# Performance work log

Hardware: AMD Instinct MI355X
Metric: run time of the kernel (lower is better)

The kernel has to match this reference:

```python
import jax, jax.numpy as jnp
import numpy as np

B, S, D = 4, 2048, 1024  # batch, seq_len, d_model (d_in == d_model)


def setup_inputs() -> dict:
    key = jax.random.key(0)
    ks = jax.random.split(key, 9)
    scale = 1.0 / np.sqrt(D)
    return {
        "q": jax.random.normal(ks[0], (B, S, D), jnp.float32),
        "k": jax.random.normal(ks[1], (B, S, D), jnp.float32),
        "v": jax.random.normal(ks[2], (B, S, D), jnp.float32),
        "Wq": jax.random.normal(ks[3], (D, D), jnp.float32) * scale,
        "bq": jnp.zeros((D,), jnp.float32),
        "Wk": jax.random.normal(ks[4], (D, D), jnp.float32) * scale,
        "bk": jnp.zeros((D,), jnp.float32),
        "Wv": jax.random.normal(ks[5], (D, D), jnp.float32) * scale,
        "bv": jnp.zeros((D,), jnp.float32),
    }


def reference(q, k, v, Wq, bq, Wk, bk, Wv, bv):
    query = q @ Wq + bq                      # [B, S, D]
    key_p = k @ Wk + bk                      # [B, S, D]
    value = v @ Wv + bv                      # [B, S, D]
    inv_sqrt_d = 1.0 / jnp.sqrt(jnp.asarray(D, query.dtype))
    scores = jnp.einsum('bqd,bkd->bqk', query, key_p) * inv_sqrt_d  # [B, S, S]
    w = jax.nn.softmax(scores, axis=-1)
    return jnp.einsum('bqk,bkd->bqd', w, value)  # [B, S, D]
```

## Files before the change

kernel.cpp:

```cpp
#include <hip/hip_runtime.h>
#include <math.h>


using short8  = __attribute__((ext_vector_type(8))) short;
using floatx4 = __attribute__((ext_vector_type(4))) float;

__device__ __forceinline__ unsigned short f2bf(float f) {
    union { float f; unsigned u; } x; x.f = f;
    return (unsigned short)((x.u + 0x8000u) >> 16);
}

__device__ __forceinline__ void gload_lds16(const unsigned short* g, unsigned short* l) {
    __builtin_amdgcn_global_load_lds(
        (const __attribute__((address_space(1))) unsigned int*)g,
        (__attribute__((address_space(3))) unsigned int*)l, 16, 0, 0);
}

__global__ __launch_bounds__(256) void prep(
    const float* __restrict__ q, const float* __restrict__ k, const float* __restrict__ v,
    const float* __restrict__ W0, const float* __restrict__ W1, const float* __restrict__ W2,
    unsigned short* __restrict__ qkvbf, unsigned short* __restrict__ Wt)
{
    __shared__ float tile[32][33];
    const int id = blockIdx.x;
    const int t  = threadIdx.x;
    if (id < 24576) {
        const int z  = id >> 13;
        const int xb = id & 8191;
        const float* x = (z == 0) ? q : (z == 1) ? k : v;
        const size_t i = ((size_t)xb * 256 + t) * 4;
        const float4 a = *(const float4*)(x + i);
        ushort4 p = { f2bf(a.x), f2bf(a.y), f2bf(a.z), f2bf(a.w) };
        *(ushort4*)(qkvbf + (size_t)z * 8192 * 1024 + i) = p;
    } else {
        const int idt = id - 24576;
        const int z  = idt >> 10;
        const int r  = idt & 1023;
        const int bx = (r & 31) * 32;
        const int by = (r >> 5) * 32;
        const float* W = (z == 0) ? W0 : (z == 1) ? W1 : W2;
        unsigned short* o = Wt + (size_t)z * 1024 * 1024;
        const int tx = t & 31;
        const int ty = (t >> 5) * 4;
        #pragma unroll
        for (int rr = 0; rr < 4; ++rr)
            tile[ty + rr][tx] = W[(size_t)(by + ty + rr) * 1024 + bx + tx];
        __syncthreads();
        #pragma unroll
        for (int rr = 0; rr < 4; ++rr)
            o[(size_t)(bx + ty + rr) * 1024 + by + tx] = f2bf(tile[tx][ty + rr]);
    }
}

#define KLOOP_BODY(gA, lda, gB, ldb, Kdim)                                        \
    for (int k0 = 0; k0 < (Kdim); k0 += 64) {                                     \
        gload_lds16(gA + k0,                    lA);                              \
        gload_lds16(gA + 64 * (lda) + k0,       lA + 2048);                       \
        gload_lds16(gA + k0 + 32,               lA + 4096);                       \
        gload_lds16(gA + 64 * (lda) + k0 + 32,  lA + 6144);                       \
        gload_lds16(gB + k0,                    lB);                              \
        gload_lds16(gB + 64 * (ldb) + k0,       lB + 2048);                       \
        gload_lds16(gB + k0 + 32,               lB + 4096);                       \
        gload_lds16(gB + 64 * (ldb) + k0 + 32,  lB + 6144);                       \
        __syncthreads();                                                          \
        _Pragma("unroll")                                                         \
        for (int h = 0; h < 2; ++h) {                                             \
            short8 af[4], bfr[4];                                                 \
            _Pragma("unroll")                                                     \
            for (int i = 0; i < 4; ++i)                                           \
                af[i] = *(const short8*)&As[h * 4096 + (wm + i * 16 + l15) * 32 + quad * 8]; \
            _Pragma("unroll")                                                     \
            for (int j = 0; j < 4; ++j)                                           \
                bfr[j] = *(const short8*)&Bs[h * 4096 + (wn + j * 16 + l15) * 32 + quad * 8]; \
            _Pragma("unroll")                                                     \
            for (int i = 0; i < 4; ++i)                                           \
                _Pragma("unroll")                                                 \
                for (int j = 0; j < 4; ++j)                                       \
                    acc[i][j] = __builtin_amdgcn_mfma_f32_16x16x32_bf16(          \
                        af[i], bfr[j], acc[i][j], 0, 0, 0);                       \
        }                                                                         \
        __syncthreads();                                                          \
    }

#define TILE_IDS                                  \
    const int t    = threadIdx.x;                 \
    const int lane = t & 63;                      \
    const int wave = t >> 6;                      \
    const int wm   = (wave & 1) * 64;             \
    const int wn   = (wave >> 1) * 64;            \
    const int l15  = lane & 15;                   \
    const int quad = lane >> 4;                   \
    const int rS = t >> 2;                        \
    const int oS = (t & 3) * 8;

__global__ __launch_bounds__(256) void proj_bf16(
    const unsigned short* __restrict__ Abf,
    const unsigned short* __restrict__ Wt,
    const float* __restrict__ bq, const float* __restrict__ bk, const float* __restrict__ bv,
    unsigned short* __restrict__ Qp, unsigned short* __restrict__ Kp,
    unsigned short* __restrict__ Vpt)
{
    const int id    = blockIdx.x;
    const int xcd   = id & 7;
    const int local = id >> 3;
    const int s     = xcd * 24 + (local >> 3);
    const int n0    = (local & 7) * 128;
    const int z     = s >> 6;
    const int m0    = (s & 63) * 128;

    const unsigned short* A = Abf + (size_t)z * 8192 * 1024;
    const unsigned short* B = Wt  + (size_t)z * 1024 * 1024;
    const float* bias = (z == 0) ? bq : (z == 1) ? bk : bv;

    __shared__ __attribute__((aligned(16))) unsigned short As[2 * 128 * 32];
    __shared__ __attribute__((aligned(16))) unsigned short Bs[2 * 128 * 32];

    TILE_IDS
    const unsigned short* gA = A + (size_t)(m0 + rS) * 1024 + oS;
    const unsigned short* gB = B + (size_t)(n0 + rS) * 1024 + oS;
    unsigned short* lA = &As[t * 8];
    unsigned short* lB = &Bs[t * 8];

    floatx4 acc[4][4] = {};

    KLOOP_BODY(gA, 1024, gB, 1024, 1024)

    #pragma unroll
    for (int j = 0; j < 4; ++j) {
        const int col = n0 + wn + j * 16 + l15;
        const float bv_ = bias[col];
        #pragma unroll
        for (int i = 0; i < 4; ++i) {
            const int row = m0 + wm + i * 16 + quad * 4;
            if (z < 2) {
                unsigned short* C = (z == 0) ? Qp : Kp;
                #pragma unroll
                for (int r = 0; r < 4; ++r)
                    C[(size_t)(row + r) * 1024 + col] = f2bf(acc[i][j][r] + bv_);
            } else {
                ushort4 p = { f2bf(acc[i][j][0] + bv_), f2bf(acc[i][j][1] + bv_),
                              f2bf(acc[i][j][2] + bv_), f2bf(acc[i][j][3] + bv_) };
                *(ushort4*)&Vpt[(size_t)col * 8192 + row] = p;
            }
        }
    }
}

__global__ __launch_bounds__(256) void scores_exp(
    const unsigned short* __restrict__ Qp,
    const unsigned short* __restrict__ Kp,
    unsigned short* __restrict__ Pexp,
    float* __restrict__ rowsum)
{
    const int id    = blockIdx.x;
    const int xcd   = id & 7;
    const int local = id >> 3;
    const int g     = xcd * 128 + local;
    const int z     = g >> 8;
    const int r_    = g & 255;
    const int cm    = r_ >> 6;
    const int rr_   = r_ & 63;
    const int cn    = rr_ >> 4;
    const int inner = rr_ & 15;
    const int m0    = (cm * 4 + (inner >> 2)) * 128;
    const int n0    = (cn * 4 + (inner & 3)) * 128;

    const unsigned short* A = Qp + (size_t)z * 2048 * 1024;
    const unsigned short* B = Kp + (size_t)z * 2048 * 1024;
    unsigned short* P = Pexp + (size_t)z * 2048 * 2048;
    float* rs = rowsum + (size_t)z * 2048;

    __shared__ __attribute__((aligned(16))) unsigned short As[2 * 128 * 32];
    __shared__ __attribute__((aligned(16))) unsigned short Bs[2 * 128 * 32];

    TILE_IDS
    const unsigned short* gA = A + (size_t)(m0 + rS) * 1024 + oS;
    const unsigned short* gB = B + (size_t)(n0 + rS) * 1024 + oS;
    unsigned short* lA = &As[t * 8];
    unsigned short* lB = &Bs[t * 8];

    floatx4 acc[4][4] = {};

    KLOOP_BODY(gA, 1024, gB, 1024, 1024)

    float sm[4][4] = {};
    #pragma unroll
    for (int i = 0; i < 4; ++i) {
        const int rowb = m0 + wm + i * 16 + quad * 4;
        #pragma unroll
        for (int j = 0; j < 4; ++j) {
            const int col = n0 + wn + j * 16 + l15;
            #pragma unroll
            for (int r = 0; r < 4; ++r) {
                const float p = __expf(acc[i][j][r] * 0.03125f);
                sm[i][r] += p;
                P[(size_t)(rowb + r) * 2048 + col] = f2bf(p);
            }
        }
    }
    #pragma unroll
    for (int i = 0; i < 4; ++i)
        #pragma unroll
        for (int r = 0; r < 4; ++r) {
            float s = sm[i][r];
            s += __shfl_xor(s, 1);
            s += __shfl_xor(s, 2);
            s += __shfl_xor(s, 4);
            s += __shfl_xor(s, 8);
            if (l15 == 0)
                atomicAdd(&rs[m0 + wm + i * 16 + quad * 4 + r], s);
        }
}

__global__ __launch_bounds__(256) void pv_norm(
    const unsigned short* __restrict__ Pexp,
    const unsigned short* __restrict__ Vpt,
    const float* __restrict__ rowsum,
    float* __restrict__ out)
{
    const int m0 = blockIdx.y * 128;
    const int n0 = blockIdx.x * 128;
    const int z  = blockIdx.z;

    const unsigned short* A = Pexp + (size_t)z * 2048 * 2048;
    const unsigned short* B = Vpt  + (size_t)z * 2048;
    const float* rs = rowsum + (size_t)z * 2048;
    float* C = out + (size_t)z * 2048 * 1024;

    __shared__ __attribute__((aligned(16))) unsigned short As[2 * 128 * 32];
    __shared__ __attribute__((aligned(16))) unsigned short Bs[2 * 128 * 32];

    TILE_IDS
    const unsigned short* gA = A + (size_t)(m0 + rS) * 2048 + oS;
    const unsigned short* gB = B + (size_t)(n0 + rS) * 8192 + oS;
    unsigned short* lA = &As[t * 8];
    unsigned short* lB = &Bs[t * 8];

    floatx4 acc[4][4] = {};

    KLOOP_BODY(gA, 2048, gB, 8192, 2048)

    #pragma unroll
    for (int i = 0; i < 4; ++i) {
        const int rowb = m0 + wm + i * 16 + quad * 4;
        float inv[4];
        #pragma unroll
        for (int r = 0; r < 4; ++r) inv[r] = 1.0f / rs[rowb + r];
        #pragma unroll
        for (int j = 0; j < 4; ++j) {
            const int col = n0 + wn + j * 16 + l15;
            #pragma unroll
            for (int r = 0; r < 4; ++r)
                C[(size_t)(rowb + r) * 1024 + col] = acc[i][j][r] * inv[r];
        }
    }
}

extern "C" void kernel_launch(void* const* d_in, const int* in_sizes, int n_in,
                              void* d_out, int out_size, void* d_ws, size_t ws_size,
                              hipStream_t stream)
{
    const float* q  = (const float*)d_in[0];
    const float* k  = (const float*)d_in[1];
    const float* v  = (const float*)d_in[2];
    const float* Wq = (const float*)d_in[3];
    const float* bq = (const float*)d_in[4];
    const float* Wk = (const float*)d_in[5];
    const float* bk = (const float*)d_in[6];
    const float* Wv = (const float*)d_in[7];
    const float* bv = (const float*)d_in[8];
    float* out = (float*)d_out;

    const int Bn = 4, S = 2048, D = 1024;
    const size_t BS = (size_t)Bn * S;

    char* w = (char*)d_ws;
    unsigned short* Wt     = (unsigned short*)(w);
    unsigned short* Qp     = (unsigned short*)(w + (6u << 20));
    unsigned short* Kp     = (unsigned short*)(w + (22u << 20));
    unsigned short* Vpt    = (unsigned short*)(w + (38u << 20));
    unsigned short* qkvbf  = (unsigned short*)(w + (54u << 20));
    unsigned short* Pexp   = (unsigned short*)(w + (54u << 20));
    float*          rowsum = (float*)(w + (86u << 20));

    const dim3 blk(256);

    hipMemsetAsync(rowsum, 0, (size_t)Bn * S * sizeof(float), stream);

    prep<<<dim3(27648), blk, 0, stream>>>(q, k, v, Wq, Wk, Wv, qkvbf, Wt);

    proj_bf16<<<dim3(1536), blk, 0, stream>>>(qkvbf, Wt, bq, bk, bv, Qp, Kp, Vpt);

    scores_exp<<<dim3(1024), blk, 0, stream>>>(Qp, Kp, Pexp, rowsum);

    pv_norm<<<dim3(D / 128, S / 128, Bn), blk, 0, stream>>>(Pexp, Vpt, rowsum, out);
}
```

Measured before the change: 316.8 us.

## Replace GEMM core with 256x256 8-wave double-buffered pipelined MFMA kernel

Replaces the 128x128 four-wave GEMM loop shared by the projection, scores and PV kernels with a 256x256 tile, eight-wave routine. It double-buffers LDS with explicit vmcnt waits and raw barriers so global-to-LDS loads overlap MFMA work, swizzles LDS columns to avoid bank conflicts, and raises wave priority around MFMA bursts. Block-to-XCD mapping is redone for the larger tiles. The larger tiles raise reuse per block, but grids shrink sharply: pv launches only 128 blocks on a 256-CU part, so occupancy and load balance may suffer. The hand-tuned wait counts are also fragile.

```diff
diff --git a/kernel.cpp b/kernel.cpp
--- a/kernel.cpp
+++ b/kernel.cpp
@@ -15,6 +15,10 @@
         (const __attribute__((address_space(1))) unsigned int*)g,
         (__attribute__((address_space(3))) unsigned int*)l, 16, 0, 0);
 }
+
+#define SBAR   __builtin_amdgcn_s_barrier()
+#define LGKM0  asm volatile("s_waitcnt lgkmcnt(0)" ::: "memory")
+#define VMW(n) asm volatile("s_waitcnt vmcnt(" #n ")" ::: "memory")
 
 __global__ __launch_bounds__(256) void prep(
     const float* __restrict__ q, const float* __restrict__ k, const float* __restrict__ v,
@@ -52,91 +56,144 @@
     }
 }
 
-#define KLOOP_BODY(gA, lda, gB, ldb, Kdim)                                        \
-    for (int k0 = 0; k0 < (Kdim); k0 += 64) {                                     \
-        gload_lds16(gA + k0,                    lA);                              \
-        gload_lds16(gA + 64 * (lda) + k0,       lA + 2048);                       \
-        gload_lds16(gA + k0 + 32,               lA + 4096);                       \
-        gload_lds16(gA + 64 * (lda) + k0 + 32,  lA + 6144);                       \
-        gload_lds16(gB + k0,                    lB);                              \
-        gload_lds16(gB + 64 * (ldb) + k0,       lB + 2048);                       \
-        gload_lds16(gB + k0 + 32,               lB + 4096);                       \
-        gload_lds16(gB + 64 * (ldb) + k0 + 32,  lB + 6144);                       \
-        __syncthreads();                                                          \
-        _Pragma("unroll")                                                         \
-        for (int h = 0; h < 2; ++h) {                                             \
-            short8 af[4], bfr[4];                                                 \
-            _Pragma("unroll")                                                     \
-            for (int i = 0; i < 4; ++i)                                           \
-                af[i] = *(const short8*)&As[h * 4096 + (wm + i * 16 + l15) * 32 + quad * 8]; \
-            _Pragma("unroll")                                                     \
-            for (int j = 0; j < 4; ++j)                                           \
-                bfr[j] = *(const short8*)&Bs[h * 4096 + (wn + j * 16 + l15) * 32 + quad * 8]; \
-            _Pragma("unroll")                                                     \
-            for (int i = 0; i < 4; ++i)                                           \
-                _Pragma("unroll")                                                 \
-                for (int j = 0; j < 4; ++j)                                       \
-                    acc[i][j] = __builtin_amdgcn_mfma_f32_16x16x32_bf16(          \
-                        af[i], bfr[j], acc[i][j], 0, 0, 0);                       \
-        }                                                                         \
-        __syncthreads();                                                          \
-    }
-
-#define TILE_IDS                                  \
-    const int t    = threadIdx.x;                 \
-    const int lane = t & 63;                      \
-    const int wave = t >> 6;                      \
-    const int wm   = (wave & 1) * 64;             \
-    const int wn   = (wave >> 1) * 64;            \
+
+#define STAGE_A(bb, ks, tt) do { \
+    const unsigned short* s_ = gA + (size_t)srow * lda + (tt) * 64 + (ks) * 32 + scol; \
+    unsigned short* d_ = lds + (bb) * 32768 + (ks) * 8192 + t512 * 8; \
+    gload_lds16(s_, d_); \
+    gload_lds16(s_ + (size_t)128 * lda, d_ + 4096); \
+} while (0)
+
+#define STAGE_B(bb, ks, tt) do { \
+    const unsigned short* s_ = gB + (size_t)srow * ldb + (tt) * 64 + (ks) * 32 + scol; \
+    unsigned short* d_ = lds + (bb) * 32768 + 16384 + (ks) * 8192 + t512 * 8; \
+    gload_lds16(s_, d_); \
+    gload_lds16(s_ + (size_t)128 * ldb, d_ + 4096); \
+} while (0)
+
+#define LDSA(bb, ks, i) (*(const short8*)&lds[(bb) * 32768 + (ks) * 8192 + (arow + (i) * 16) * 32 + rslot])
+#define LDSB(bb, ks, j) (*(const short8*)&lds[(bb) * 32768 + 16384 + (ks) * 8192 + (brow + (j) * 16) * 32 + rslot])
+
+#define MFMA16(IB) do { \
+    __builtin_amdgcn_s_setprio(1); \
+    _Pragma("unroll") \
+    for (int i_ = 0; i_ < 4; ++i_) \
+        _Pragma("unroll") \
+        for (int j_ = 0; j_ < 4; ++j_) \
+            acc[(IB) + i_][j_] = __builtin_amdgcn_mfma_f32_16x16x32_bf16( \
+                af[i_], bf[j_], acc[(IB) + i_][j_], 0, 0, 0); \
+    __builtin_amdgcn_s_setprio(0); \
+} while (0)
+
+__device__ __forceinline__ void gemm8ph(
+    const unsigned short* __restrict__ gA, int lda,
+    const unsigned short* __restrict__ gB, int ldb,
+    int nt, unsigned short* lds, floatx4 (&acc)[8][4])
+{
+    const int t512 = threadIdx.x;
+    const int lane = t512 & 63;
+    const int wave = t512 >> 6;
+    const int wr   = wave >> 2;
+    const int wc   = wave & 3;
+    const int l15  = lane & 15;
+    const int quad = lane >> 4;
+    const int srow = t512 >> 2;
+    const int scol = ((t512 & 3) ^ ((t512 >> 3) & 3)) * 8;
+    const int rslot = (quad ^ ((l15 >> 1) & 3)) * 8;
+    const int arow = wr * 128 + l15;
+    const int brow = wc * 64 + l15;
+
+    short8 af[4], bf[4];
+
+    STAGE_B(0, 0, 0); STAGE_A(0, 0, 0); STAGE_B(0, 1, 0); STAGE_A(0, 1, 0);
+    STAGE_B(1, 0, 1); STAGE_A(1, 0, 1); STAGE_B(1, 1, 1);
+    VMW(10);
+    SBAR;
+
+    int b = 0;
+    for (int t = 0; t < nt; ++t, b ^= 1) {
+        #pragma unroll
+        for (int j = 0; j < 4; ++j) bf[j] = LDSB(b, 0, j);
+        #pragma unroll
+        for (int i = 0; i < 4; ++i) af[i] = LDSA(b, 0, i);
+        if (t + 1 < nt) STAGE_A(b ^ 1, 1, t + 1);
+        SBAR; LGKM0;
+        MFMA16(0);
+        SBAR;
+        #pragma unroll
+        for (int i = 0; i < 4; ++i) af[i] = LDSA(b, 0, i + 4);
+        if (t + 2 < nt) STAGE_B(b, 0, t + 2);
+        SBAR; LGKM0;
+        MFMA16(4);
+        if (t == nt - 1)      VMW(0);
+        else if (t == nt - 2) VMW(8);
+        else                  VMW(10);
+        SBAR;
+        #pragma unroll
+        for (int j = 0; j < 4; ++j) bf[j] = LDSB(b, 1, j);
+        #pragma unroll
+        for (int i = 0; i < 4; ++i) af[i] = LDSA(b, 1, i);
+        if (t + 2 < nt) STAGE_A(b, 0, t + 2);
+        SBAR; LGKM0;
+        MFMA16(0);
+        SBAR;
+        #pragma unroll
+        for (int i = 0; i < 4; ++i) af[i] = LDSA(b, 1, i + 4);
+        if (t + 2 < nt) STAGE_B(b, 1, t + 2);
+        SBAR; LGKM0;
+        MFMA16(4);
+        if (t + 1 < nt) {
+            if (t + 1 == nt - 1) VMW(4);
+            else                 VMW(10);
+            SBAR;
+        }
+    }
+}
+
+#define EPI_IDS                                   \
+    const int tt   = threadIdx.x;                 \
+    const int lane = tt & 63;                     \
+    const int wave = tt >> 6;                     \
+    const int wr   = wave >> 2;                   \
+    const int wc   = wave & 3;                    \
     const int l15  = lane & 15;                   \
-    const int quad = lane >> 4;                   \
-    const int rS = t >> 2;                        \
-    const int oS = (t & 3) * 8;
-
-__global__ __launch_bounds__(256) void proj_bf16(
+    const int quad = lane >> 4;
+
+__global__ __launch_bounds__(512, 2) void proj8(
     const unsigned short* __restrict__ Abf,
     const unsigned short* __restrict__ Wt,
     const float* __restrict__ bq, const float* __restrict__ bk, const float* __restrict__ bv,
     unsigned short* __restrict__ Qp, unsigned short* __restrict__ Kp,
     unsigned short* __restrict__ Vpt)
 {
-    const int id    = blockIdx.x;
-    const int xcd   = id & 7;
-    const int local = id >> 3;
-    const int s     = xcd * 24 + (local >> 3);
-    const int n0    = (local & 7) * 128;
-    const int z     = s >> 6;
-    const int m0    = (s & 63) * 128;
-
-    const unsigned short* A = Abf + (size_t)z * 8192 * 1024;
-    const unsigned short* B = Wt  + (size_t)z * 1024 * 1024;
+    __shared__ __attribute__((aligned(16))) unsigned short lds[65536];
+    const int id = blockIdx.x;
+    const int g  = (id & 7) * 48 + (id >> 3);
+    const int z  = g >> 7;
+    const int r  = g & 127;
+    const int m0 = (r >> 2) * 256;
+    const int n0 = (r & 3) * 256;
+
+    const unsigned short* gA = Abf + (size_t)z * 8192 * 1024 + (size_t)m0 * 1024;
+    const unsigned short* gB = Wt  + (size_t)z * 1024 * 1024 + (size_t)n0 * 1024;
+
+    floatx4 acc[8][4] = {};
+    gemm8ph(gA, 1024, gB, 1024, 16, lds, acc);
+
+    EPI_IDS
     const float* bias = (z == 0) ? bq : (z == 1) ? bk : bv;
-
-    __shared__ __attribute__((aligned(16))) unsigned short As[2 * 128 * 32];
-    __shared__ __attribute__((aligned(16))) unsigned short Bs[2 * 128 * 32];
-
-    TILE_IDS
-    const unsigned short* gA = A + (size_t)(m0 + rS) * 1024 + oS;
-    const unsigned short* gB = B + (size_t)(n0 + rS) * 1024 + oS;
-    unsigned short* lA = &As[t * 8];
-    unsigned short* lB = &Bs[t * 8];
-
-    floatx4 acc[4][4] = {};
-
-    KLOOP_BODY(gA, 1024, gB, 1024, 1024)
-
     #pragma unroll
     for (int j = 0; j < 4; ++j) {
-        const int col = n0 + wn + j * 16 + l15;
+        const int col = n0 + wc * 64 + j * 16 + l15;
         const float bv_ = bias[col];
         #pragma unroll
-        for (int i = 0; i < 4; ++i) {
-            const int row = m0 + wm + i * 16 + quad * 4;
+        for (int i = 0; i < 8; ++i) {
+            const int row = m0 + wr * 128 + i * 16 + quad * 4;
             if (z < 2) {
                 unsigned short* C = (z == 0) ? Qp : Kp;
                 #pragma unroll
-                for (int r = 0; r < 4; ++r)
-                    C[(size_t)(row + r) * 1024 + col] = f2bf(acc[i][j][r] + bv_);
+                for (int r2 = 0; r2 < 4; ++r2)
+                    C[(size_t)(row + r2) * 1024 + col] = f2bf(acc[i][j][r2] + bv_);
             } else {
                 ushort4 p = { f2bf(acc[i][j][0] + bv_), f2bf(acc[i][j][1] + bv_),
                               f2bf(acc[i][j][2] + bv_), f2bf(acc[i][j][3] + bv_) };
@@ -146,112 +203,91 @@
     }
 }
 
-__global__ __launch_bounds__(256) void scores_exp(
+__global__ __launch_bounds__(512, 2) void scores8(
     const unsigned short* __restrict__ Qp,
     const unsigned short* __restrict__ Kp,
     unsigned short* __restrict__ Pexp,
     float* __restrict__ rowsum)
 {
-    const int id    = blockIdx.x;
-    const int xcd   = id & 7;
-    const int local = id >> 3;
-    const int g     = xcd * 128 + local;
-    const int z     = g >> 8;
-    const int r_    = g & 255;
-    const int cm    = r_ >> 6;
-    const int rr_   = r_ & 63;
-    const int cn    = rr_ >> 4;
-    const int inner = rr_ & 15;
-    const int m0    = (cm * 4 + (inner >> 2)) * 128;
-    const int n0    = (cn * 4 + (inner & 3)) * 128;
-
-    const unsigned short* A = Qp + (size_t)z * 2048 * 1024;
-    const unsigned short* B = Kp + (size_t)z * 2048 * 1024;
+    __shared__ __attribute__((aligned(16))) unsigned short lds[65536];
+    const int id = blockIdx.x;
+    const int g  = (id & 7) * 32 + (id >> 3);
+    const int z  = g >> 6;
+    const int r  = g & 63;
+    const int m0 = (r >> 3) * 256;
+    const int n0 = (r & 7) * 256;
+
+    const unsigned short* gA = Qp + (size_t)z * 2048 * 1024 + (size_t)m0 * 1024;
+    const unsigned short* gB = Kp + (size_t)z * 2048 * 1024 + (size_t)n0 * 1024;
+
+    floatx4 acc[8][4] = {};
+    gemm8ph(gA, 1024, gB, 1024, 16, lds, acc);
+
+    EPI_IDS
     unsigned short* P = Pexp + (size_t)z * 2048 * 2048;
     float* rs = rowsum + (size_t)z * 2048;
-
-    __shared__ __attribute__((aligned(16))) unsigned short As[2 * 128 * 32];
-    __shared__ __attribute__((aligned(16))) unsigned short Bs[2 * 128 * 32];
-
-    TILE_IDS
-    const unsigned short* gA = A + (size_t)(m0 + rS) * 1024 + oS;
-    const unsigned short* gB = B + (size_t)(n0 + rS) * 1024 + oS;
-    unsigned short* lA = &As[t * 8];
-    unsigned short* lB = &Bs[t * 8];
-
-    floatx4 acc[4][4] = {};
-
-    KLOOP_BODY(gA, 1024, gB, 1024, 1024)
-
-    float sm[4][4] = {};
     #pragma unroll
-    for (int i = 0; i < 4; ++i) {
-        const int rowb = m0 + wm + i * 16 + quad * 4;
+    for (int i = 0; i < 8; ++i) {
+        const int rowb = m0 + wr * 128 + i * 16 + quad * 4;
+        float sm[4] = {0.f, 0.f, 0.f, 0.f};
         #pragma unroll
         for (int j = 0; j < 4; ++j) {
-            const int col = n0 + wn + j * 16 + l15;
+            const int col = n0 + wc * 64 + j * 16 + l15;
             #pragma unroll
-            for (int r = 0; r < 4; ++r) {
-                const float p = __expf(acc[i][j][r] * 0.03125f);
-                sm[i][r] += p;
-                P[(size_t)(rowb + r) * 2048 + col] = f2bf(p);
+            for (int r2 = 0; r2 < 4; ++r2) {
+                const float p = __expf(acc[i][j][r2] * 0.03125f);
+                sm[r2] += p;
+                P[(size_t)(rowb + r2) * 2048 + col] = f2bf(p);
             }
         }
-    }
-    #pragma unroll
-    for (int i = 0; i < 4; ++i)
-        #pragma unroll
-        for (int r = 0; r < 4; ++r) {
-            float s = sm[i][r];
+        #pragma unroll
+        for (int r2 = 0; r2 < 4; ++r2) {
+            float s = sm[r2];
             s += __shfl_xor(s, 1);
             s += __shfl_xor(s, 2);
             s += __shfl_xor(s, 4);
             s += __shfl_xor(s, 8);
             if (l15 == 0)
-                atomicAdd(&rs[m0 + wm + i * 16 + quad * 4 + r], s);
-        }
-}
-
-__global__ __launch_bounds__(256) void pv_norm(
+                atomicAdd(&rs[rowb + r2], s);
+        }
+    }
+}
+
+__global__ __launch_bounds__(512, 2) void pv8(
     const unsigned short* __restrict__ Pexp,
     const unsigned short* __restrict__ Vpt,
     const float* __restrict__ rowsum,
     float* __restrict__ out)
 {
-    const int m0 = blockIdx.y * 128;
-    const int n0 = blockIdx.x * 128;
-    const int z  = blockIdx.z;
-
-    const unsigned short* A = Pexp + (size_t)z * 2048 * 2048;
-    const unsigned short* B = Vpt  + (size_t)z * 2048;
+    __shared__ __attribute__((aligned(16))) unsigned short lds[65536];
+    const int id = blockIdx.x;
+    const int g  = (id & 7) * 16 + (id >> 3);
+    const int z  = g >> 5;
+    const int r  = g & 31;
+    const int m0 = (r >> 2) * 256;
+    const int n0 = (r & 3) * 256;
+
+    const unsigned short* gA = Pexp + (size_t)z * 2048 * 2048 + (size_t)m0 * 2048;
+    const unsigned short* gB = Vpt  + (size_t)n0 * 8192 + (size_t)z * 2048;
+
+    floatx4 acc[8][4] = {};
+    gemm8ph(gA, 2048, gB, 8192, 32, lds, acc);
+
+    EPI_IDS
     const float* rs = rowsum + (size_t)z * 2048;
     float* C = out + (size_t)z * 2048 * 1024;
-
-    __shared__ __attribute__((aligned(16))) unsigned short As[2 * 128 * 32];
-    __shared__ __attribute__((aligned(16))) unsigned short Bs[2 * 128 * 32];
-
-    TILE_IDS
-    const unsigned short* gA = A + (size_t)(m0 + rS) * 2048 + oS;
-    const unsigned short* gB = B + (size_t)(n0 + rS) * 8192 + oS;
-    unsigned short* lA = &As[t * 8];
-    unsigned short* lB = &Bs[t * 8];
-
-    floatx4 acc[4][4] = {};
-
-    KLOOP_BODY(gA, 2048, gB, 8192, 2048)
-
     #pragma unroll
-    for (int i = 0; i < 4; ++i) {
-        const int rowb = m0 + wm + i * 16 + quad * 4;
+    for (int i = 0; i < 8; ++i) {
+        const int rowb = m0 + wr * 128 + i * 16 + quad * 4;
         float inv[4];
         #pragma unroll
-        for (int r = 0; r < 4; ++r) inv[r] = 1.0f / rs[rowb + r];
+        for (int r2 = 0; r2 < 4; ++r2) inv[r2] = 1.0f / rs[rowb + r2];
         #pragma unroll
         for (int j = 0; j < 4; ++j) {
-            const int col = n0 + wn + j * 16 + l15;
+            const int col = n0 + wc * 64 + j * 16 + l15;
             #pragma unroll
-            for (int r = 0; r < 4; ++r)
-                C[(size_t)(rowb + r) * 1024 + col] = acc[i][j][r] * inv[r];
+            for (int r2 = 0; r2 < 4; ++r2)
+                C[(size_t)(rowb + r2) * 1024 + col] = acc[i][j][r2] * inv[r2];
         }
     }
 }
@@ -271,8 +307,7 @@
     const float* bv = (const float*)d_in[8];
     float* out = (float*)d_out;
 
-    const int Bn = 4, S = 2048, D = 1024;
-    const size_t BS = (size_t)Bn * S;
+    const int Bn = 4, S = 2048;
 
     char* w = (char*)d_ws;
     unsigned short* Wt     = (unsigned short*)(w);
@@ -283,15 +318,13 @@
     unsigned short* Pexp   = (unsigned short*)(w + (54u << 20));
     float*          rowsum = (float*)(w + (86u << 20));
 
-    const dim3 blk(256);
-
     hipMemsetAsync(rowsum, 0, (size_t)Bn * S * sizeof(float), stream);
 
-    prep<<<dim3(27648), blk, 0, stream>>>(q, k, v, Wq, Wk, Wv, qkvbf, Wt);
-
-    proj_bf16<<<dim3(1536), blk, 0, stream>>>(qkvbf, Wt, bq, bk, bv, Qp, Kp, Vpt);
-
-    scores_exp<<<dim3(1024), blk, 0, stream>>>(Qp, Kp, Pexp, rowsum);
-
-    pv_norm<<<dim3(D / 128, S / 128, Bn), blk, 0, stream>>>(Pexp, Vpt, rowsum, out);
-}
+    prep<<<dim3(27648), dim3(256), 0, stream>>>(q, k, v, Wq, Wk, Wv, qkvbf, Wt);
+
+    proj8<<<dim3(384), dim3(512), 0, stream>>>(qkvbf, Wt, bq, bk, bv, Qp, Kp, Vpt);
+
+    scores8<<<dim3(256), dim3(512), 0, stream>>>(Qp, Kp, Pexp, rowsum);
+
+    pv8<<<dim3(128), dim3(512), 0, stream>>>(Pexp, Vpt, rowsum, out);
+}
```

Result: slower. 331.8 us (+4.7%).
